# Kernel optimization log

Hardware: AMD Instinct MI355X
Metric: run time of the kernel (lower is better)

The kernel has to match this reference:

```python
import jax, jax.numpy as jnp
import numpy as np

N = 50000          # num_nodes
D = 32             # latent_dim
E2 = 800000        # undirected edge pairs; E = 2*E2 directed edges
STEP = 1.0         # step_size


def setup_inputs() -> dict:
    key = jax.random.key(0)
    k1, k2, k3, k4 = jax.random.split(key, 4)
    # Build a symmetric edge list so every edge (s,t) has its reverse (t,s).
    rng = np.random.default_rng(0)
    src = rng.integers(0, N, size=E2)
    dst = rng.integers(0, N, size=E2)
    edge_index = jnp.asarray(
        np.stack([np.concatenate([src, dst]), np.concatenate([dst, src])]),
        dtype=jnp.int32)                                   # [2, 2*E2]
    # reverse-edge index: edge e in first half <-> e+E2 in second half
    right_idx = jnp.asarray(
        np.concatenate([np.arange(E2) + E2, np.arange(E2)]), dtype=jnp.int32)
    x = jax.random.normal(k1, (N, D), dtype=jnp.float32)
    sheaf_W = jax.random.normal(k2, (1, 2 * D), dtype=jnp.float32) * 0.1
    lin_W = jax.random.normal(k3, (D, D), dtype=jnp.float32) * 0.1
    lin_b = jax.random.normal(k4, (D,), dtype=jnp.float32) * 0.1
    return {"x": x, "sheaf_W": sheaf_W, "lin_W": lin_W, "lin_b": lin_b,
            "edge_index": edge_index, "right_idx": right_idx}


def reference(x, sheaf_W, lin_W, lin_b, edge_index, right_idx):
    row, col = edge_index[0], edge_index[1]
    # predict_restriction_maps: maps = tanh(W_s [x_row ; x_col])  -> [E, 1]
    xe = jnp.concatenate([x[row], x[col]], axis=1)          # [E, 2D]
    maps = jnp.tanh(xe @ sheaf_W.T)                         # [E, 1]
    # build_laplacian (left_idx is identity)
    non_diag = -(maps * maps[right_idx])                    # [E, 1]
    diag_maps = jax.ops.segment_sum(maps ** 2, row, num_segments=N)  # [N, 1]
    d_si = (diag_maps + 1.0) ** -0.5                        # [N, 1]
    norm_maps = d_si[row] * non_diag * d_si[col]            # [E, 1]
    diag = (d_si * diag_maps * d_si)[:, 0]                  # [N]
    # y = linear(x); sparse Laplacian matmul: L @ y
    y = x @ lin_W.T + lin_b                                 # [N, D]
    Ly = diag[:, None] * y + jax.ops.segment_sum(
        norm_maps * y[col], row, num_segments=N)            # [N, D]
    return x - STEP * Ly
```

## Files before the change

kernel.cpp:

```cpp
#include <hip/hip_runtime.h>

#define D 32
#define GBITS 6
#define GSIZE 64
#define BLK 256
#define PPC 4096
#define IPT 16
#define CAP 2560

typedef unsigned long long ull;

static __device__ __forceinline__ unsigned short f2h(float f) {
    _Float16 h = (_Float16)f;
    return __builtin_bit_cast(unsigned short, h);
}
static __device__ __forceinline__ float h2f(unsigned short u) {
    return (float)__builtin_bit_cast(_Float16, u);
}
static __device__ __forceinline__ float ftanh(float u) {
    u = fminf(fmaxf(u, -15.f), 15.f);
    float e = __expf(2.f * u);
    return (e - 1.f) / (e + 1.f);
}

__global__ void k_pre_hist(const float* __restrict__ x,
                           const float* __restrict__ sheafW,
                           const float* __restrict__ linW,
                           const float* __restrict__ linb,
                           const int* __restrict__ ei,
                           float2* __restrict__ ab,
                           unsigned short* __restrict__ y_h,
                           int* __restrict__ bhist,
                           int N, int E2, int E, int nbN, int nblkH, int NBG) {
    if (blockIdx.x < nbN) {
        __shared__ float sW[D * D];
        __shared__ float sB[D];
        __shared__ float sS[2 * D];
        for (int i = threadIdx.x; i < D * D; i += blockDim.x) sW[i] = linW[i];
        if (threadIdx.x < D) sB[threadIdx.x] = linb[threadIdx.x];
        if (threadIdx.x < 2 * D) sS[threadIdx.x] = sheafW[threadIdx.x];
        __syncthreads();

        int n = blockIdx.x * blockDim.x + threadIdx.x;
        if (n >= N) return;

        float xv[D];
        const float4* xp = reinterpret_cast<const float4*>(x + (size_t)n * D);
#pragma unroll
        for (int i = 0; i < D / 4; ++i) {
            float4 v = xp[i];
            xv[4 * i + 0] = v.x; xv[4 * i + 1] = v.y;
            xv[4 * i + 2] = v.z; xv[4 * i + 3] = v.w;
        }

        float av = 0.f, bv = 0.f;
#pragma unroll
        for (int d = 0; d < D; ++d) { av += xv[d] * sS[d]; bv += xv[d] * sS[D + d]; }
        ab[n] = make_float2(av, bv);

        unsigned short yh[D];
#pragma unroll
        for (int j = 0; j < D; ++j) {
            float s = sB[j];
#pragma unroll
            for (int d = 0; d < D; ++d) s += xv[d] * sW[j * D + d];
            yh[j] = f2h(s);
        }
        uint4* dst = reinterpret_cast<uint4*>(y_h + (size_t)n * D);
        const uint4* src = reinterpret_cast<const uint4*>(yh);
#pragma unroll
        for (int q = 0; q < D / 8; ++q) dst[q] = src[q];
    } else {
        __shared__ int hist[1024];
        int blk = blockIdx.x - nbN;
        for (int i = threadIdx.x; i < NBG; i += BLK) hist[i] = 0;
        __syncthreads();
        int base = blk * PPC;
#pragma unroll
        for (int k = 0; k < IPT; ++k) {
            int i = base + k * BLK + threadIdx.x;
            if (i < E2) {
                int s = ei[i];
                int t = ei[E + i];
                atomicAdd(&hist[s >> GBITS], 1);
                atomicAdd(&hist[t >> GBITS], 1);
            }
        }
        __syncthreads();
        for (int i = threadIdx.x; i < NBG; i += BLK)
            bhist[(size_t)i * nblkH + blk] = hist[i];
    }
}

__global__ void k_scanA(int* __restrict__ data, int* __restrict__ bsum, int M) {
    __shared__ int s[256];
    int t = threadIdx.x;
    int i = blockIdx.x * 256 + t;
    int v = (i < M) ? data[i] : 0;
    s[t] = v;
    __syncthreads();
#pragma unroll
    for (int o = 1; o < 256; o <<= 1) {
        int tmp = (t >= o) ? s[t - o] : 0;
        __syncthreads();
        s[t] += tmp;
        __syncthreads();
    }
    if (i < M) data[i] = s[t] - v;
    if (t == 255) bsum[blockIdx.x] = s[255];
}

__global__ void k_scanB(int* __restrict__ data, int NB) {
    __shared__ int s[1024];
    int t = threadIdx.x;
    int per = (NB + 1023) >> 10;
    int beg = t * per;
    int end_ = min(beg + per, NB);
    int sum = 0;
    for (int i = beg; i < end_; ++i) sum += data[i];
    s[t] = sum;
    __syncthreads();
#pragma unroll
    for (int o = 1; o < 1024; o <<= 1) {
        int tmp = (t >= o) ? s[t - o] : 0;
        __syncthreads();
        s[t] += tmp;
        __syncthreads();
    }
    int run = s[t] - sum;
    for (int i = beg; i < end_; ++i) { int v = data[i]; data[i] = run; run += v; }
}

__global__ void k_scatter(const int* __restrict__ ei,
                          const float2* __restrict__ ab,
                          const int* __restrict__ bhist,
                          const int* __restrict__ bsum,
                          ull* __restrict__ binned,
                          int E2, int E, int nblkH, int NBG) {
    __shared__ int cursor[1024];
    for (int i = threadIdx.x; i < NBG; i += BLK) {
        int idx = i * nblkH + blockIdx.x;
        cursor[i] = bhist[idx] + bsum[idx >> 8];
    }
    __syncthreads();
    int base = blockIdx.x * PPC;
#pragma unroll
    for (int k = 0; k < IPT; ++k) {
        int i = base + k * BLK + threadIdx.x;
        if (i < E2) {
            int s = ei[i];
            int t = ei[E + i];
            float2 as = ab[s], at = ab[t];
            float m  = ftanh(as.x + at.y);
            float mr = ftanh(at.x + as.y);
            ull hm = f2h(m), hmr = f2h(mr);
            int pos = atomicAdd(&cursor[s >> GBITS], 1);
            binned[pos] = ((ull)(unsigned)s << 48) | ((ull)(unsigned)t << 32) | (hm << 16) | hmr;
            int pos2 = atomicAdd(&cursor[t >> GBITS], 1);
            binned[pos2] = ((ull)(unsigned)t << 48) | ((ull)(unsigned)s << 32) | (hmr << 16) | hm;
        }
    }
}

__global__ void k_diag(const ull* __restrict__ binned,
                       const int* __restrict__ bhist,
                       const int* __restrict__ bsum,
                       float* __restrict__ dsi, float* __restrict__ diag2,
                       int E, int nblkH, int NBG, int N) {
    __shared__ float rdiag[GSIZE];
    __shared__ int sgs[2];
    int g = blockIdx.x, t = threadIdx.x;
    if (t < GSIZE) rdiag[t] = 0.f;
    if (t < 2) {
        int gg = g + t;
        if (gg < NBG) {
            int idx = gg * nblkH;
            sgs[t] = bhist[idx] + bsum[idx >> 8];
        } else sgs[t] = E;
    }
    __syncthreads();
    int gstart = sgs[0], gend = sgs[1];
    for (int k = gstart + t; k < gend; k += BLK) {
        ull it = binned[k];
        int r = (int)(it >> 48) & (GSIZE - 1);
        float m = h2f((unsigned short)((it >> 16) & 0xFFFF));
        atomicAdd(&rdiag[r], m * m);
    }
    __syncthreads();
    int n0 = g << GBITS;
    if (t < GSIZE) {
        int n = n0 + t;
        if (n < N) {
            float dm = rdiag[t];
            float ds = rsqrtf(dm + 1.0f);
            dsi[n] = ds;
            diag2[n] = dm * ds * ds;
        }
    }
}

__global__ __launch_bounds__(512) void k_gather_fused(
        const ull* __restrict__ binned,
        const int* __restrict__ bhist,
        const int* __restrict__ bsum,
        const unsigned short* __restrict__ y_h,
        const float* __restrict__ x,
        const float* __restrict__ dsi,
        const float* __restrict__ diag2,
        float* __restrict__ out,
        int E, int nblkH, int NBG, int N) {
    __shared__ unsigned int sortedw[CAP];
    __shared__ int rhist[GSIZE];
    __shared__ int rbase[GSIZE];
    __shared__ int cur[GSIZE];
    __shared__ float sds[GSIZE];
    __shared__ float sdg[GSIZE];
    __shared__ int ss[GSIZE];
    __shared__ int sgs[2];
    int g = blockIdx.x, t = threadIdx.x;
    int n0 = g << GBITS;
    if (t < GSIZE) {
        rhist[t] = 0;
        int n = n0 + t;
        if (n < N) { sds[t] = dsi[n]; sdg[t] = diag2[n]; }
    }
    if (t < 2) {
        int gg = g + t;
        if (gg < NBG) {
            int idx = gg * nblkH;
            sgs[t] = bhist[idx] + bsum[idx >> 8];
        } else sgs[t] = E;
    }
    __syncthreads();
    int gstart = sgs[0];
    int cnt = min(sgs[1] - gstart, CAP);

    for (int k = t; k < cnt; k += 512) {
        ull it = binned[gstart + k];
        atomicAdd(&rhist[(int)(it >> 48) & (GSIZE - 1)], 1);
    }
    __syncthreads();

    int v = (t < GSIZE) ? rhist[t] : 0;
    if (t < GSIZE) ss[t] = v;
    __syncthreads();
#pragma unroll
    for (int o = 1; o < GSIZE; o <<= 1) {
        int tmp = 0;
        if (t < GSIZE && t >= o) tmp = ss[t - o];
        __syncthreads();
        if (t < GSIZE) ss[t] += tmp;
        __syncthreads();
    }
    if (t < GSIZE) {
        int ex = ss[t] - v;
        rbase[t] = ex;
        cur[t] = ex;
    }
    __syncthreads();

    for (int k = t; k < cnt; k += 512) {
        ull it = binned[gstart + k];
        int r = (int)(it >> 48) & (GSIZE - 1);
        unsigned int c = (unsigned int)((it >> 32) & 0xFFFF);
        float w = h2f((unsigned short)((it >> 16) & 0xFFFF)) *
                  h2f((unsigned short)(it & 0xFFFF)) * dsi[c];
        int pos = atomicAdd(&cur[r], 1);
        sortedw[pos] = (c << 16) | (unsigned int)f2h(w);
    }
    __syncthreads();

    int hw = t >> 5;
    int lane = t & 31;
    int rows = min(GSIZE, N - n0);
    for (int r = hw; r < rows; r += 16) {
        int beg = rbase[r];
        int end_ = beg + rhist[r];
        float acc = 0.f;
        int k = beg;
        for (; k + 4 <= end_; k += 4) {
            unsigned int e0 = sortedw[k + 0];
            unsigned int e1 = sortedw[k + 1];
            unsigned int e2 = sortedw[k + 2];
            unsigned int e3 = sortedw[k + 3];
            float v0 = h2f(y_h[(size_t)(e0 >> 16) * D + lane]);
            float v1 = h2f(y_h[(size_t)(e1 >> 16) * D + lane]);
            float v2 = h2f(y_h[(size_t)(e2 >> 16) * D + lane]);
            float v3 = h2f(y_h[(size_t)(e3 >> 16) * D + lane]);
            acc += h2f((unsigned short)(e0 & 0xFFFF)) * v0;
            acc += h2f((unsigned short)(e1 & 0xFFFF)) * v1;
            acc += h2f((unsigned short)(e2 & 0xFFFF)) * v2;
            acc += h2f((unsigned short)(e3 & 0xFFFF)) * v3;
        }
        for (; k < end_; ++k) {
            unsigned int e = sortedw[k];
            acc += h2f((unsigned short)(e & 0xFFFF)) *
                   h2f(y_h[(size_t)(e >> 16) * D + lane]);
        }
        size_t p = (size_t)(n0 + r) * D + lane;
        float yown = h2f(y_h[p]);
        out[p] = x[p] - sdg[r] * yown + sds[r] * acc;
    }
}

extern "C" void kernel_launch(void* const* d_in, const int* in_sizes, int n_in,
                              void* d_out, int out_size, void* d_ws, size_t ws_size,
                              hipStream_t stream) {
    const float* x      = (const float*)d_in[0];
    const float* sheafW = (const float*)d_in[1];
    const float* linW   = (const float*)d_in[2];
    const float* linb   = (const float*)d_in[3];
    const int*   ei     = (const int*)d_in[4];

    int N  = in_sizes[0] / D;
    int E  = in_sizes[4] / 2;
    int E2 = E / 2;

    int NBG   = (N + GSIZE - 1) >> GBITS;
    int nblkH = (E2 + PPC - 1) / PPC;
    int MH    = NBG * nblkH;
    int nblkA = (MH + 255) / 256;

    char* wp = (char*)d_ws;
    ull*    binned = (ull*)wp;    wp += (size_t)E * 8;
    float2* ab     = (float2*)wp; wp += (size_t)N * 8;
    float*  dsi    = (float*)wp;  wp += (size_t)N * 4;
    float*  diag2  = (float*)wp;  wp += (size_t)N * 4;
    unsigned short* y_h = (unsigned short*)wp; wp += (size_t)N * D * 2;
    int*    bhist  = (int*)wp;    wp += (size_t)MH * 4;
    int*    bsumA  = (int*)wp;    wp += (size_t)nblkA * 4;

    float* out = (float*)d_out;

    int nbN = (N + BLK - 1) / BLK;

    k_pre_hist<<<nbN + nblkH, BLK, 0, stream>>>(x, sheafW, linW, linb, ei, ab, y_h,
                                                bhist, N, E2, E, nbN, nblkH, NBG);
    k_scanA<<<nblkA, 256, 0, stream>>>(bhist, bsumA, MH);
    k_scanB<<<1, 1024, 0, stream>>>(bsumA, nblkA);
    k_scatter<<<nblkH, BLK, 0, stream>>>(ei, ab, bhist, bsumA, binned, E2, E, nblkH, NBG);
    k_diag<<<NBG, BLK, 0, stream>>>(binned, bhist, bsumA, dsi, diag2, E, nblkH, NBG, N);
    k_gather_fused<<<NBG, 512, 0, stream>>>(binned, bhist, bsumA, y_h, x, dsi, diag2,
                                            out, E, nblkH, NBG, N);
}
```

Baseline: 91.37 us.

## Compute per-row histogram and offsets in diag kernel; enlarge scatter/pre blocks

```diff
diff --git a/kernel.cpp b/kernel.cpp
--- a/kernel.cpp
+++ b/kernel.cpp
@@ -3,9 +3,9 @@
 #define D 32
 #define GBITS 6
 #define GSIZE 64
-#define BLK 256
+#define BLK 1024
 #define PPC 4096
-#define IPT 16
+#define IPT 4
 #define CAP 2560
 
 typedef unsigned long long ull;
@@ -23,7 +23,8 @@
     return (e - 1.f) / (e + 1.f);
 }
 
-__global__ void k_pre_hist(const float* __restrict__ x,
+__global__ __launch_bounds__(BLK) void k_pre_hist(
+                           const float* __restrict__ x,
                            const float* __restrict__ sheafW,
                            const float* __restrict__ linW,
                            const float* __restrict__ linb,
@@ -38,7 +39,7 @@
         __shared__ float sS[2 * D];
         for (int i = threadIdx.x; i < D * D; i += blockDim.x) sW[i] = linW[i];
         if (threadIdx.x < D) sB[threadIdx.x] = linb[threadIdx.x];
-        if (threadIdx.x < 2 * D) sS[threadIdx.x] = sheafW[threadIdx.x];
+        else if (threadIdx.x >= D && threadIdx.x < 3 * D) sS[threadIdx.x - D] = sheafW[threadIdx.x - D];
         __syncthreads();
 
         int n = blockIdx.x * blockDim.x + threadIdx.x;
@@ -131,7 +132,8 @@
     for (int i = beg; i < end_; ++i) { int v = data[i]; data[i] = run; run += v; }
 }
 
-__global__ void k_scatter(const int* __restrict__ ei,
+__global__ __launch_bounds__(BLK) void k_scatter(
+                          const int* __restrict__ ei,
                           const float2* __restrict__ ab,
                           const int* __restrict__ bhist,
                           const int* __restrict__ bsum,
@@ -166,11 +168,14 @@
                        const int* __restrict__ bhist,
                        const int* __restrict__ bsum,
                        float* __restrict__ dsi, float* __restrict__ diag2,
+                       int* __restrict__ rbase_g, int* __restrict__ rcnt_g,
                        int E, int nblkH, int NBG, int N) {
     __shared__ float rdiag[GSIZE];
+    __shared__ int rhist[GSIZE];
+    __shared__ int ss[GSIZE];
     __shared__ int sgs[2];
     int g = blockIdx.x, t = threadIdx.x;
-    if (t < GSIZE) rdiag[t] = 0.f;
+    if (t < GSIZE) { rdiag[t] = 0.f; rhist[t] = 0; }
     if (t < 2) {
         int gg = g + t;
         if (gg < NBG) {
@@ -180,13 +185,25 @@
     }
     __syncthreads();
     int gstart = sgs[0], gend = sgs[1];
-    for (int k = gstart + t; k < gend; k += BLK) {
+    for (int k = gstart + t; k < gend; k += 256) {
         ull it = binned[k];
         int r = (int)(it >> 48) & (GSIZE - 1);
         float m = h2f((unsigned short)((it >> 16) & 0xFFFF));
         atomicAdd(&rdiag[r], m * m);
-    }
-    __syncthreads();
+        atomicAdd(&rhist[r], 1);
+    }
+    __syncthreads();
+    int v = (t < GSIZE) ? rhist[t] : 0;
+    if (t < GSIZE) ss[t] = v;
+    __syncthreads();
+#pragma unroll
+    for (int o = 1; o < GSIZE; o <<= 1) {
+        int tmp = 0;
+        if (t < GSIZE && t >= o) tmp = ss[t - o];
+        __syncthreads();
+        if (t < GSIZE) ss[t] += tmp;
+        __syncthreads();
+    }
     int n0 = g << GBITS;
     if (t < GSIZE) {
         int n = n0 + t;
@@ -195,6 +212,8 @@
             float ds = rsqrtf(dm + 1.0f);
             dsi[n] = ds;
             diag2[n] = dm * ds * ds;
+            rbase_g[n] = ss[t] - v;
+            rcnt_g[n] = v;
         }
     }
 }
@@ -207,57 +226,38 @@
         const float* __restrict__ x,
         const float* __restrict__ dsi,
         const float* __restrict__ diag2,
+        const int* __restrict__ rbase_g,
+        const int* __restrict__ rcnt_g,
         float* __restrict__ out,
         int E, int nblkH, int NBG, int N) {
     __shared__ unsigned int sortedw[CAP];
-    __shared__ int rhist[GSIZE];
     __shared__ int rbase[GSIZE];
+    __shared__ int rcnt[GSIZE];
     __shared__ int cur[GSIZE];
     __shared__ float sds[GSIZE];
     __shared__ float sdg[GSIZE];
-    __shared__ int ss[GSIZE];
-    __shared__ int sgs[2];
+    __shared__ int sgs[1];
     int g = blockIdx.x, t = threadIdx.x;
     int n0 = g << GBITS;
     if (t < GSIZE) {
-        rhist[t] = 0;
         int n = n0 + t;
-        if (n < N) { sds[t] = dsi[n]; sdg[t] = diag2[n]; }
-    }
-    if (t < 2) {
-        int gg = g + t;
-        if (gg < NBG) {
-            int idx = gg * nblkH;
-            sgs[t] = bhist[idx] + bsum[idx >> 8];
-        } else sgs[t] = E;
+        if (n < N) {
+            sds[t] = dsi[n]; sdg[t] = diag2[n];
+            int rb = rbase_g[n];
+            rbase[t] = rb; cur[t] = rb; rcnt[t] = rcnt_g[n];
+        } else { rbase[t] = 0; cur[t] = 0; rcnt[t] = 0; }
+    }
+    if (t == 0) {
+        int idx = g * nblkH;
+        sgs[0] = bhist[idx] + bsum[idx >> 8];
     }
     __syncthreads();
     int gstart = sgs[0];
-    int cnt = min(sgs[1] - gstart, CAP);
-
-    for (int k = t; k < cnt; k += 512) {
-        ull it = binned[gstart + k];
-        atomicAdd(&rhist[(int)(it >> 48) & (GSIZE - 1)], 1);
-    }
-    __syncthreads();
-
-    int v = (t < GSIZE) ? rhist[t] : 0;
-    if (t < GSIZE) ss[t] = v;
-    __syncthreads();
-#pragma unroll
-    for (int o = 1; o < GSIZE; o <<= 1) {
-        int tmp = 0;
-        if (t < GSIZE && t >= o) tmp = ss[t - o];
-        __syncthreads();
-        if (t < GSIZE) ss[t] += tmp;
-        __syncthreads();
-    }
-    if (t < GSIZE) {
-        int ex = ss[t] - v;
-        rbase[t] = ex;
-        cur[t] = ex;
-    }
-    __syncthreads();
+    int cnt = 0;
+    {
+        int lastn = min(n0 + GSIZE, N) - 1;
+        if (lastn >= n0) cnt = min(rbase[lastn - n0] + rcnt[lastn - n0], CAP);
+    }
 
     for (int k = t; k < cnt; k += 512) {
         ull it = binned[gstart + k];
@@ -275,7 +275,7 @@
     int rows = min(GSIZE, N - n0);
     for (int r = hw; r < rows; r += 16) {
         int beg = rbase[r];
-        int end_ = beg + rhist[r];
+        int end_ = beg + rcnt[r];
         float acc = 0.f;
         int k = beg;
         for (; k + 4 <= end_; k += 4) {
@@ -329,6 +329,8 @@
     unsigned short* y_h = (unsigned short*)wp; wp += (size_t)N * D * 2;
     int*    bhist  = (int*)wp;    wp += (size_t)MH * 4;
     int*    bsumA  = (int*)wp;    wp += (size_t)nblkA * 4;
+    int*    rbase_g= (int*)wp;    wp += (size_t)N * 4;
+    int*    rcnt_g = (int*)wp;    wp += (size_t)N * 4;
 
     float* out = (float*)d_out;
 
@@ -339,7 +341,8 @@
     k_scanA<<<nblkA, 256, 0, stream>>>(bhist, bsumA, MH);
     k_scanB<<<1, 1024, 0, stream>>>(bsumA, nblkA);
     k_scatter<<<nblkH, BLK, 0, stream>>>(ei, ab, bhist, bsumA, binned, E2, E, nblkH, NBG);
-    k_diag<<<NBG, BLK, 0, stream>>>(binned, bhist, bsumA, dsi, diag2, E, nblkH, NBG, N);
+    k_diag<<<NBG, 256, 0, stream>>>(binned, bhist, bsumA, dsi, diag2, rbase_g, rcnt_g,
+                                    E, nblkH, NBG, N);
     k_gather_fused<<<NBG, 512, 0, stream>>>(binned, bhist, bsumA, y_h, x, dsi, diag2,
-                                            out, E, nblkH, NBG, N);
-}
+                                            rbase_g, rcnt_g, out, E, nblkH, NBG, N);
+}
```

Measured after the change: 98.07 us. +7.3%, slower.
